# Performance work log

Hardware: AMD Instinct MI355X
Metric: run time of the kernel (lower is better)

Reference implementation:

```python
import jax, jax.numpy as jnp
import numpy as np

N, K, C_IN, OUT = 65536, 16, 64, 64
MID = OUT  # mid_planes = out_planes // 1
S = 8      # share_planes
EPS = 1e-5


def _bn(x, gamma, beta, mean, var):
    # Keras BatchNormalization (inference) over the last (channel) axis.
    return (x - mean) * jax.lax.rsqrt(var + EPS) * gamma + beta


def setup_inputs() -> dict:
    key = jax.random.key(0)
    ks = jax.random.split(key, 12)
    d = {
        'point': jax.random.normal(ks[0], (N, 3), jnp.float32),
        'feat': jax.random.normal(ks[1], (N, C_IN), jnp.float32),
        'idx': jax.random.randint(ks[2], (N, K), 0, N, jnp.int32),
        # linear_q / linear_k / linear_v
        'Wq': jax.random.normal(ks[3], (C_IN, MID), jnp.float32) * 0.05,
        'bq': jnp.zeros((MID,), jnp.float32),
        'Wk': jax.random.normal(ks[4], (C_IN, MID), jnp.float32) * 0.05,
        'bk': jnp.zeros((MID,), jnp.float32),
        'Wv': jax.random.normal(ks[5], (C_IN, OUT), jnp.float32) * 0.05,
        'bv': jnp.zeros((OUT,), jnp.float32),
        # linear_p: Dense(3) -> BN -> ReLU -> Dense(out)
        'p_w1': jax.random.normal(ks[6], (3, 3), jnp.float32) * 0.5,
        'p_b1': jnp.zeros((3,), jnp.float32),
        'p_bn_g': jnp.ones((3,), jnp.float32),
        'p_bn_b': jnp.zeros((3,), jnp.float32),
        'p_bn_m': jnp.zeros((3,), jnp.float32),
        'p_bn_v': jnp.ones((3,), jnp.float32),
        'p_w2': jax.random.normal(ks[7], (3, OUT), jnp.float32) * 0.1,
        'p_b2': jnp.zeros((OUT,), jnp.float32),
        # linear_w: BN -> ReLU -> Dense(mid//s) -> BN -> ReLU -> Dense(out//s)
        'w_bn1_g': jnp.ones((MID,), jnp.float32),
        'w_bn1_b': jnp.zeros((MID,), jnp.float32),
        'w_bn1_m': jnp.zeros((MID,), jnp.float32),
        'w_bn1_v': jnp.ones((MID,), jnp.float32),
        'w_w1': jax.random.normal(ks[8], (MID, MID // S), jnp.float32) * 0.05,
        'w_b1': jnp.zeros((MID // S,), jnp.float32),
        'w_bn2_g': jnp.ones((MID // S,), jnp.float32),
        'w_bn2_b': jnp.zeros((MID // S,), jnp.float32),
        'w_bn2_m': jnp.zeros((MID // S,), jnp.float32),
        'w_bn2_v': jnp.ones((MID // S,), jnp.float32),
        'w_w2': jax.random.normal(ks[9], (MID // S, OUT // S), jnp.float32) * 0.1,
        'w_b2': jnp.zeros((OUT // S,), jnp.float32),
    }
    return d


def reference(point, feat, idx, Wq, bq, Wk, bk, Wv, bv,
              p_w1, p_b1, p_bn_g, p_bn_b, p_bn_m, p_bn_v, p_w2, p_b2,
              w_bn1_g, w_bn1_b, w_bn1_m, w_bn1_v, w_w1, w_b1,
              w_bn2_g, w_bn2_b, w_bn2_m, w_bn2_v, w_w2, w_b2):
    n = point.shape[0]
    feat_q = feat @ Wq + bq                       # (n, mid)
    feat_k = feat @ Wk + bk                       # (n, mid)
    feat_v = feat @ Wv + bv                       # (n, out)
    # queryandgroup: KNN gather + relative positions
    g_xyz = point[idx] - point[:, None, :]        # (n, k, 3)
    g_k = feat_k[idx]                             # (n, k, mid)
    g_v = feat_v[idx]                             # (n, k, out)
    # linear_p MLP on relative positions
    p = g_xyz @ p_w1 + p_b1
    p = jax.nn.relu(_bn(p, p_bn_g, p_bn_b, p_bn_m, p_bn_v))
    p = p @ p_w2 + p_b2                           # (n, k, out)
    # sum over out_planes//mid_planes (= 1) groups, kept for faithfulness
    pr = p.reshape(n, K, OUT // MID, MID).sum(axis=2)  # (n, k, mid)
    # subtraction attention scores
    w = g_k - feat_q[:, None, :] + pr             # (n, k, mid)
    w = jax.nn.relu(_bn(w, w_bn1_g, w_bn1_b, w_bn1_m, w_bn1_v))
    w = w @ w_w1 + w_b1                           # (n, k, mid//s)
    w = jax.nn.relu(_bn(w, w_bn2_g, w_bn2_b, w_bn2_m, w_bn2_v))
    w = w @ w_w2 + w_b2                           # (n, k, out//s)
    # NOTE: original uses Softmax(axis=-1) -> over the out//share channel axis
    w = jax.nn.softmax(w, axis=-1)
    # grouped weighted sum over neighbors
    v = (g_v + p).reshape(n, K, S, OUT // S)      # (n, k, s, out//s)
    out = (v * w[:, :, None, :]).sum(axis=1)      # (n, s, out//s)
    return out.reshape(n, OUT)
```

## Files before the change

kernel.cpp:

```cpp
#include <hip/hip_runtime.h>

typedef unsigned short u16;
typedef unsigned int   u32;
typedef float f32x2 __attribute__((ext_vector_type(2)));

__device__ __forceinline__ u16 f2b(float f) {
    u32 u = __float_as_uint(f);
    return (u16)((u + 0x7fffu + ((u >> 16) & 1u)) >> 16);
}
__device__ __forceinline__ u32 pack2f(float a, float b) {
    return (u32)f2b(a) | ((u32)f2b(b) << 16);
}
__device__ __forceinline__ f32x2 unpk2(u32 w) {
    f32x2 r;
    r[0] = __uint_as_float(w << 16);
    r[1] = __uint_as_float(w & 0xffff0000u);
    return r;
}
__device__ __forceinline__ int permc(int c) { return ((c & 7) << 3) | (c >> 3); }
__device__ __forceinline__ f32x2 bc2(float x) { f32x2 r; r[0] = x; r[1] = x; return r; }
__device__ __forceinline__ f32x2 mk2(float a, float b) { f32x2 r; r[0] = a; r[1] = b; return r; }

__device__ __forceinline__ void dot2bf(float& c, u32 a, u32 b) {
    asm("v_dot2_f32_bf16 %0, %1, %2, %0" : "+v"(c) : "v"(a), "v"(b));
}
__device__ __forceinline__ u32 cvtpk(float lo, float hi) {
    u32 r;
    asm("v_cvt_pk_bf16_f32 %0, %1, %2" : "=v"(r) : "v"(lo), "v"(hi));
    return r;
}

template<int CTRL>
__device__ __forceinline__ float dppf(float x) {
    return __int_as_float(__builtin_amdgcn_update_dpp(0, __float_as_int(x), CTRL, 0xf, 0xf, true));
}
__device__ __forceinline__ float gsum8(float x) {
    x += dppf<0xB1>(x);
    x += dppf<0x4E>(x);
    x += dppf<0x141>(x);
    return x;
}
__device__ __forceinline__ float gmax8(float x) {
    x = fmaxf(x, dppf<0xB1>(x));
    x = fmaxf(x, dppf<0x4E>(x));
    x = fmaxf(x, dppf<0x141>(x));
    return x;
}

__global__ __launch_bounds__(256) void qkv_kernel(
    const float* __restrict__ feat,
    const float* __restrict__ Wq, const float* __restrict__ bq,
    const float* __restrict__ Wk, const float* __restrict__ bk,
    const float* __restrict__ Wv, const float* __restrict__ bv,
    u16* __restrict__ qt, u16* __restrict__ kvt)
{
    __shared__ u32 wpk[3][32][64];
    __shared__ u32 fpk[32][132];
    const int t = threadIdx.x;
    const int rowbase = blockIdx.x * 128;

    {
        const float* Ws[3] = {Wq, Wk, Wv};
#pragma unroll
        for (int mm = 0; mm < 3; mm++) {
            for (int e = t; e < 512; e += 256) {
                int ip = e >> 4, c4 = (e & 15) * 4;
                float4 wa = *(const float4*)&Ws[mm][(2 * ip) * 64 + c4];
                float4 wb = *(const float4*)&Ws[mm][(2 * ip + 1) * 64 + c4];
                wpk[mm][ip][permc(c4 + 0)] = pack2f(wa.x, wb.x);
                wpk[mm][ip][permc(c4 + 1)] = pack2f(wa.y, wb.y);
                wpk[mm][ip][permc(c4 + 2)] = pack2f(wa.z, wb.z);
                wpk[mm][ip][permc(c4 + 3)] = pack2f(wa.w, wb.w);
            }
        }
    }
    for (int e = t; e < 2048; e += 256) {
        int r = e >> 4, ip2 = (e & 15) * 2;
        float4 v = *(const float4*)&feat[(size_t)(rowbase + r) * 64 + ip2 * 2];
        fpk[ip2][r]     = pack2f(v.x, v.y);
        fpk[ip2 + 1][r] = pack2f(v.z, v.w);
    }
    __syncthreads();

    const int rg = t >> 3;
    const int q8 = t & 7;
    const int c0 = q8 * 8;

    float acc[3][4][8];
    {
        const float* Bs[3] = {bq, bk, bv};
#pragma unroll
        for (int m = 0; m < 3; m++)
#pragma unroll
            for (int x = 0; x < 8; x++) {
                float b = Bs[m][x * 8 + q8];
#pragma unroll
                for (int r = 0; r < 4; r++) acc[m][r][x] = b;
            }
    }

#pragma unroll 2
    for (int ip = 0; ip < 32; ip++) {
        uint4 f4 = *(const uint4*)&fpk[ip][rg * 4];
        u32 fr[4] = {f4.x, f4.y, f4.z, f4.w};
#pragma unroll
        for (int m = 0; m < 3; m++) {
            uint4 wv0 = *(const uint4*)&wpk[m][ip][c0];
            uint4 wv1 = *(const uint4*)&wpk[m][ip][c0 + 4];
            u32 wc[8] = {wv0.x, wv0.y, wv0.z, wv0.w, wv1.x, wv1.y, wv1.z, wv1.w};
#pragma unroll
            for (int r = 0; r < 4; r++)
#pragma unroll
                for (int x = 0; x < 8; x++)
                    dot2bf(acc[m][r][x], fr[r], wc[x]);
        }
    }

#pragma unroll
    for (int r = 0; r < 4; r++) {
        int row = rowbase + rg * 4 + r;
        uint4 oq, ok, ov;
        oq.x = cvtpk(acc[0][r][0], acc[0][r][1]); oq.y = cvtpk(acc[0][r][2], acc[0][r][3]);
        oq.z = cvtpk(acc[0][r][4], acc[0][r][5]); oq.w = cvtpk(acc[0][r][6], acc[0][r][7]);
        ok.x = cvtpk(acc[1][r][0], acc[1][r][1]); ok.y = cvtpk(acc[1][r][2], acc[1][r][3]);
        ok.z = cvtpk(acc[1][r][4], acc[1][r][5]); ok.w = cvtpk(acc[1][r][6], acc[1][r][7]);
        ov.x = cvtpk(acc[2][r][0], acc[2][r][1]); ov.y = cvtpk(acc[2][r][2], acc[2][r][3]);
        ov.z = cvtpk(acc[2][r][4], acc[2][r][5]); ov.w = cvtpk(acc[2][r][6], acc[2][r][7]);
        *(uint4*)&qt [(size_t)row * 64 + c0]       = oq;
        *(uint4*)&kvt[(size_t)row * 128 + c0]      = ok;
        *(uint4*)&kvt[(size_t)row * 128 + 64 + c0] = ov;
    }
}

__global__ __launch_bounds__(256) void attn_kernel(
    const float* __restrict__ point,
    const int*   __restrict__ idx,
    const u16*   __restrict__ qt,
    const u16*   __restrict__ kvt,
    const float* __restrict__ p_w1,   const float* __restrict__ p_b1,
    const float* __restrict__ p_bn_g, const float* __restrict__ p_bn_b,
    const float* __restrict__ p_bn_m, const float* __restrict__ p_bn_v,
    const float* __restrict__ p_w2,   const float* __restrict__ p_b2,
    const float* __restrict__ w_bn1_g, const float* __restrict__ w_bn1_b,
    const float* __restrict__ w_bn1_m, const float* __restrict__ w_bn1_v,
    const float* __restrict__ w_w1,    const float* __restrict__ w_b1,
    const float* __restrict__ w_bn2_g, const float* __restrict__ w_bn2_b,
    const float* __restrict__ w_bn2_m, const float* __restrict__ w_bn2_v,
    const float* __restrict__ w_w2,    const float* __restrict__ w_b2,
    float* __restrict__ out)
{
    const int t  = threadIdx.x;
    const int l8 = t & 7;
    const int n  = blockIdx.x * 32 + (t >> 3);
    const float EPS = 1e-5f;

    float pw1[9];
#pragma unroll
    for (int i = 0; i < 9; i++) pw1[i] = p_w1[i];
    float pb1b[3], pbs[3], pbh[3];
#pragma unroll
    for (int a = 0; a < 3; a++) {
        float s = p_bn_g[a] * rsqrtf(p_bn_v[a] + EPS);
        pb1b[a] = p_b1[a];
        pbs[a]  = s;
        pbh[a]  = p_bn_b[a] - p_bn_m[a] * s;
    }
    float b2s[8], b2hh[8];
#pragma unroll
    for (int h = 0; h < 8; h++) {
        float s = w_bn2_g[h] * rsqrtf(w_bn2_v[h] + EPS);
        b2s[h]  = s;
        b2hh[h] = (w_bn2_b[h] - w_bn2_m[h] * s) + w_b1[h] * s;
    }

    f32x2 P0[4], P1[4], P2[4], PB[4];
#pragma unroll
    for (int p = 0; p < 4; p++) {
        int ce = 16 * p + l8, co = ce + 8;
        P0[p] = mk2(p_w2[ce],       p_w2[co]);
        P1[p] = mk2(p_w2[64 + ce],  p_w2[64 + co]);
        P2[p] = mk2(p_w2[128 + ce], p_w2[128 + co]);
        PB[p] = mk2(p_b2[ce],       p_b2[co]);
    }
    u32 W1pk[4][8];
#pragma unroll
    for (int p = 0; p < 4; p++) {
        int ce = 16 * p + l8, co = ce + 8;
        float4 e0 = *(const float4*)&w_w1[ce * 8];
        float4 e1 = *(const float4*)&w_w1[ce * 8 + 4];
        float4 o0 = *(const float4*)&w_w1[co * 8];
        float4 o1 = *(const float4*)&w_w1[co * 8 + 4];
        W1pk[p][0] = pack2f(e0.x, o0.x); W1pk[p][1] = pack2f(e0.y, o0.y);
        W1pk[p][2] = pack2f(e0.z, o0.z); W1pk[p][3] = pack2f(e0.w, o0.w);
        W1pk[p][4] = pack2f(e1.x, o1.x); W1pk[p][5] = pack2f(e1.y, o1.y);
        W1pk[p][6] = pack2f(e1.z, o1.z); W1pk[p][7] = pack2f(e1.w, o1.w);
    }
    u32 ww2pk[4];
#pragma unroll
    for (int i = 0; i < 4; i++)
        ww2pk[i] = pack2f(w_w2[(2 * i) * 8 + l8], w_w2[(2 * i + 1) * 8 + l8]);
    const float wb2l = w_b2[l8];

    f32x2 s2[4], qh2[4];
    {
        uint4 qr = *(const uint4*)&qt[(size_t)n * 64 + l8 * 8];
        const u32* qw = (const u32*)&qr;
#pragma unroll
        for (int p = 0; p < 4; p++) {
            int ce = 16 * p + l8, co = ce + 8;
            float se = w_bn1_g[ce] * rsqrtf(w_bn1_v[ce] + EPS);
            float so = w_bn1_g[co] * rsqrtf(w_bn1_v[co] + EPS);
            float he = w_bn1_b[ce] - w_bn1_m[ce] * se;
            float ho = w_bn1_b[co] - w_bn1_m[co] * so;
            f32x2 q2 = unpk2(qw[p]);
            s2[p]  = mk2(se, so);
            qh2[p] = mk2(he - q2[0] * se, ho - q2[1] * so);
        }
    }

    const float px = point[n * 3], py = point[n * 3 + 1], pz = point[n * 3 + 2];
    f32x2 acc2[4];
#pragma unroll
    for (int p = 0; p < 4; p++) acc2[p] = mk2(0.f, 0.f);

    const int ib = n * 16;
    int j_nxt = idx[ib];
    const u16* kp0 = kvt + (size_t)j_nxt * 128 + l8 * 8;
    uint4 kr = *(const uint4*)kp0;
    uint4 vr = *(const uint4*)(kp0 + 64);
    float2 jxy = *(const float2*)&point[j_nxt * 3];
    float  jz  = point[j_nxt * 3 + 2];
    j_nxt = idx[ib + 1];

#pragma unroll 4
    for (int kk = 0; kk < 16; kk++) {
        int i2 = kk + 2;
        int j_n2 = idx[ib + (i2 < 16 ? i2 : 15)];
        const u16* kpn = kvt + (size_t)j_nxt * 128 + l8 * 8;
        uint4 krn = *(const uint4*)kpn;
        uint4 vrn = *(const uint4*)(kpn + 64);
        float2 jxyn = *(const float2*)&point[j_nxt * 3];
        float  jzn  = point[j_nxt * 3 + 2];

        float dx = jxy.x - px, dy = jxy.y - py, dz = jz - pz;
        float t0 = fmaxf(0.f, fmaf(fmaf(dz, pw1[6], fmaf(dy, pw1[3], fmaf(dx, pw1[0], pb1b[0]))), pbs[0], pbh[0]));
        float t1 = fmaxf(0.f, fmaf(fmaf(dz, pw1[7], fmaf(dy, pw1[4], fmaf(dx, pw1[1], pb1b[1]))), pbs[1], pbh[1]));
        float t2 = fmaxf(0.f, fmaf(fmaf(dz, pw1[8], fmaf(dy, pw1[5], fmaf(dx, pw1[2], pb1b[2]))), pbs[2], pbh[2]));
        f32x2 tp0 = bc2(t0), tp1 = bc2(t1), tp2 = bc2(t2);

        const u32* kw = (const u32*)&kr;
        float partial[8];
#pragma unroll
        for (int h = 0; h < 8; h++) partial[h] = 0.f;
        f32x2 pjs[4];

#pragma unroll
        for (int p = 0; p < 4; p++) {
            f32x2 pj = PB[p] + tp0 * P0[p] + tp1 * P1[p] + tp2 * P2[p];
            pjs[p] = pj;
            f32x2 kf = unpk2(kw[p]);
            f32x2 w2 = (kf + pj) * s2[p] + qh2[p];
            u32 wpk_ = cvtpk(fmaxf(w2[0], 0.f), fmaxf(w2[1], 0.f));
#pragma unroll
            for (int h = 0; h < 8; h++) dot2bf(partial[h], wpk_, W1pk[p][h]);
        }
#pragma unroll
        for (int h = 0; h < 8; h++) partial[h] = gsum8(partial[h]);

        float wb[8];
#pragma unroll
        for (int h = 0; h < 8; h++) wb[h] = fmaxf(0.f, fmaf(partial[h], b2s[h], b2hh[h]));
        float y = wb2l;
#pragma unroll
        for (int i = 0; i < 4; i++) dot2bf(y, cvtpk(wb[2 * i], wb[2 * i + 1]), ww2pk[i]);

        float mx = gmax8(y);
        float e  = __expf(y - mx);
        float ssum = gsum8(e);
        float sm = e * __builtin_amdgcn_rcpf(ssum);
        f32x2 sm2 = bc2(sm);

        const u32* vw = (const u32*)&vr;
#pragma unroll
        for (int p = 0; p < 4; p++) {
            f32x2 vp = unpk2(vw[p]) + pjs[p];
            acc2[p] += sm2 * vp;
        }

        kr = krn; vr = vrn; jxy = jxyn; jz = jzn; j_nxt = j_n2;
    }

#pragma unroll
    for (int p = 0; p < 4; p++) {
        out[(size_t)n * 64 + 16 * p + l8]     = acc2[p][0];
        out[(size_t)n * 64 + 16 * p + 8 + l8] = acc2[p][1];
    }
}

extern "C" void kernel_launch(void* const* d_in, const int* in_sizes, int n_in,
                              void* d_out, int out_size, void* d_ws, size_t ws_size,
                              hipStream_t stream)
{
    const float* point   = (const float*)d_in[0];
    const float* feat    = (const float*)d_in[1];
    const int*   idx     = (const int*)d_in[2];
    const float* Wq      = (const float*)d_in[3];
    const float* bq      = (const float*)d_in[4];
    const float* Wk      = (const float*)d_in[5];
    const float* bk      = (const float*)d_in[6];
    const float* Wv      = (const float*)d_in[7];
    const float* bv      = (const float*)d_in[8];
    const float* p_w1    = (const float*)d_in[9];
    const float* p_b1    = (const float*)d_in[10];
    const float* p_bn_g  = (const float*)d_in[11];
    const float* p_bn_b  = (const float*)d_in[12];
    const float* p_bn_m  = (const float*)d_in[13];
    const float* p_bn_v  = (const float*)d_in[14];
    const float* p_w2    = (const float*)d_in[15];
    const float* p_b2    = (const float*)d_in[16];
    const float* w_bn1_g = (const float*)d_in[17];
    const float* w_bn1_b = (const float*)d_in[18];
    const float* w_bn1_m = (const float*)d_in[19];
    const float* w_bn1_v = (const float*)d_in[20];
    const float* w_w1    = (const float*)d_in[21];
    const float* w_b1    = (const float*)d_in[22];
    const float* w_bn2_g = (const float*)d_in[23];
    const float* w_bn2_b = (const float*)d_in[24];
    const float* w_bn2_m = (const float*)d_in[25];
    const float* w_bn2_v = (const float*)d_in[26];
    const float* w_w2    = (const float*)d_in[27];
    const float* w_b2    = (const float*)d_in[28];
    float* out = (float*)d_out;

    const int N = in_sizes[0] / 3;

    u16* kvt = (u16*)d_ws;
    u16* qt  = (u16*)d_ws + (size_t)N * 128;

    qkv_kernel<<<N / 128, 256, 0, stream>>>(feat, Wq, bq, Wk, bk, Wv, bv, qt, kvt);
    attn_kernel<<<N / 32, 256, 0, stream>>>(point, idx, qt, kvt,
                                            p_w1, p_b1, p_bn_g, p_bn_b, p_bn_m, p_bn_v, p_w2, p_b2,
                                            w_bn1_g, w_bn1_b, w_bn1_m, w_bn1_v, w_w1, w_b1,
                                            w_bn2_g, w_bn2_b, w_bn2_m, w_bn2_v, w_w2, w_b2,
                                            out);
}
```

Baseline: 86.32 us.

## Replace per-head butterfly reductions with transpose-reduce and vectorize neighbor index loads

Eight separate gsum8 reductions over the 8-lane group are replaced by a DPP transpose-reduce. Each lane ends up holding one head's sum, which takes seven DPP adds instead of twenty-four. The W1 and W2 weights are pre-permuted per lane (phi8 xor lane) so that the reduced values and the DPP-broadcast values line up with the correct heads for the second dot product. Neighbor indices are now loaded as int4 vectors and the loop is fully unrolled through a lambda, which cuts scalar index loads but may raise register pressure.

```diff
diff --git a/kernel.cpp b/kernel.cpp
--- a/kernel.cpp
+++ b/kernel.cpp
@@ -46,6 +46,7 @@
     x = fmaxf(x, dppf<0x141>(x));
     return x;
 }
+__device__ __forceinline__ int phi8(int r) { return (r < 4) ? r : (r ^ 3); }
 
 __global__ __launch_bounds__(256) void qkv_kernel(
     const float* __restrict__ feat,
@@ -165,13 +166,6 @@
         pbs[a]  = s;
         pbh[a]  = p_bn_b[a] - p_bn_m[a] * s;
     }
-    float b2s[8], b2hh[8];
-#pragma unroll
-    for (int h = 0; h < 8; h++) {
-        float s = w_bn2_g[h] * rsqrtf(w_bn2_v[h] + EPS);
-        b2s[h]  = s;
-        b2hh[h] = (w_bn2_b[h] - w_bn2_m[h] * s) + w_b1[h] * s;
-    }
 
     f32x2 P0[4], P1[4], P2[4], PB[4];
 #pragma unroll
@@ -186,19 +180,25 @@
 #pragma unroll
     for (int p = 0; p < 4; p++) {
         int ce = 16 * p + l8, co = ce + 8;
-        float4 e0 = *(const float4*)&w_w1[ce * 8];
-        float4 e1 = *(const float4*)&w_w1[ce * 8 + 4];
-        float4 o0 = *(const float4*)&w_w1[co * 8];
-        float4 o1 = *(const float4*)&w_w1[co * 8 + 4];
-        W1pk[p][0] = pack2f(e0.x, o0.x); W1pk[p][1] = pack2f(e0.y, o0.y);
-        W1pk[p][2] = pack2f(e0.z, o0.z); W1pk[p][3] = pack2f(e0.w, o0.w);
-        W1pk[p][4] = pack2f(e1.x, o1.x); W1pk[p][5] = pack2f(e1.y, o1.y);
-        W1pk[p][6] = pack2f(e1.z, o1.z); W1pk[p][7] = pack2f(e1.w, o1.w);
-    }
-    u32 ww2pk[4];
-#pragma unroll
-    for (int i = 0; i < 4; i++)
-        ww2pk[i] = pack2f(w_w2[(2 * i) * 8 + l8], w_w2[(2 * i + 1) * 8 + l8]);
+#pragma unroll
+        for (int r = 0; r < 8; r++) {
+            int hh = phi8(r) ^ l8;
+            W1pk[p][r] = pack2f(w_w1[ce * 8 + hh], w_w1[co * 8 + hh]);
+        }
+    }
+    float b2s_l, b2hh_l;
+    {
+        float s = w_bn2_g[l8] * rsqrtf(w_bn2_v[l8] + EPS);
+        b2s_l  = s;
+        b2hh_l = (w_bn2_b[l8] - w_bn2_m[l8] * s) + w_b1[l8] * s;
+    }
+    u32 ww2xpk[4];
+#pragma unroll
+    for (int i = 0; i < 4; i++) {
+        int h0 = phi8(2 * i)     ^ l8;
+        int h1 = phi8(2 * i + 1) ^ l8;
+        ww2xpk[i] = pack2f(w_w2[h0 * 8 + l8], w_w2[h1 * 8 + l8]);
+    }
     const float wb2l = w_b2[l8];
 
     f32x2 s2[4], qh2[4];
@@ -223,24 +223,16 @@
 #pragma unroll
     for (int p = 0; p < 4; p++) acc2[p] = mk2(0.f, 0.f);
 
-    const int ib = n * 16;
-    int j_nxt = idx[ib];
-    const u16* kp0 = kvt + (size_t)j_nxt * 128 + l8 * 8;
-    uint4 kr = *(const uint4*)kp0;
-    uint4 vr = *(const uint4*)(kp0 + 64);
-    float2 jxy = *(const float2*)&point[j_nxt * 3];
-    float  jz  = point[j_nxt * 3 + 2];
-    j_nxt = idx[ib + 1];
-
-#pragma unroll 4
-    for (int kk = 0; kk < 16; kk++) {
-        int i2 = kk + 2;
-        int j_n2 = idx[ib + (i2 < 16 ? i2 : 15)];
-        const u16* kpn = kvt + (size_t)j_nxt * 128 + l8 * 8;
+    uint4 kr, vr;
+    float2 jxy;
+    float  jz;
+
+    auto proc = [&](int jn) {
+        const u16* kpn = kvt + (size_t)jn * 128 + l8 * 8;
         uint4 krn = *(const uint4*)kpn;
         uint4 vrn = *(const uint4*)(kpn + 64);
-        float2 jxyn = *(const float2*)&point[j_nxt * 3];
-        float  jzn  = point[j_nxt * 3 + 2];
+        float2 jxyn = *(const float2*)&point[jn * 3];
+        float  jzn  = point[jn * 3 + 2];
 
         float dx = jxy.x - px, dy = jxy.y - py, dz = jz - pz;
         float t0 = fmaxf(0.f, fmaf(fmaf(dz, pw1[6], fmaf(dy, pw1[3], fmaf(dx, pw1[0], pb1b[0]))), pbs[0], pbh[0]));
@@ -249,9 +241,9 @@
         f32x2 tp0 = bc2(t0), tp1 = bc2(t1), tp2 = bc2(t2);
 
         const u32* kw = (const u32*)&kr;
-        float partial[8];
-#pragma unroll
-        for (int h = 0; h < 8; h++) partial[h] = 0.f;
+        float part[8];
+#pragma unroll
+        for (int h = 0; h < 8; h++) part[h] = 0.f;
         f32x2 pjs[4];
 
 #pragma unroll
@@ -262,17 +254,28 @@
             f32x2 w2 = (kf + pj) * s2[p] + qh2[p];
             u32 wpk_ = cvtpk(fmaxf(w2[0], 0.f), fmaxf(w2[1], 0.f));
 #pragma unroll
-            for (int h = 0; h < 8; h++) dot2bf(partial[h], wpk_, W1pk[p][h]);
-        }
-#pragma unroll
-        for (int h = 0; h < 8; h++) partial[h] = gsum8(partial[h]);
-
-        float wb[8];
-#pragma unroll
-        for (int h = 0; h < 8; h++) wb[h] = fmaxf(0.f, fmaf(partial[h], b2s[h], b2hh[h]));
+            for (int r = 0; r < 8; r++) dot2bf(part[r], wpk_, W1pk[p][r]);
+        }
+        part[0] += dppf<0xB1>(part[1]);
+        part[2] += dppf<0xB1>(part[3]);
+        part[4] += dppf<0xB1>(part[5]);
+        part[6] += dppf<0xB1>(part[7]);
+        part[0] += dppf<0x4E>(part[2]);
+        part[4] += dppf<0x4E>(part[6]);
+        part[0] += dppf<0x141>(part[4]);
+        float wbl = fmaxf(0.f, fmaf(part[0], b2s_l, b2hh_l));
+        float u1 = dppf<0xB1>(wbl);
+        float u2 = dppf<0x4E>(wbl);
+        float u3 = dppf<0x4E>(u1);
+        float u4 = dppf<0x141>(wbl);
+        float u5 = dppf<0x141>(u1);
+        float u6 = dppf<0x141>(u2);
+        float u7 = dppf<0x141>(u3);
         float y = wb2l;
-#pragma unroll
-        for (int i = 0; i < 4; i++) dot2bf(y, cvtpk(wb[2 * i], wb[2 * i + 1]), ww2pk[i]);
+        dot2bf(y, cvtpk(wbl, u1), ww2xpk[0]);
+        dot2bf(y, cvtpk(u2, u3), ww2xpk[1]);
+        dot2bf(y, cvtpk(u4, u5), ww2xpk[2]);
+        dot2bf(y, cvtpk(u6, u7), ww2xpk[3]);
 
         float mx = gmax8(y);
         float e  = __expf(y - mx);
@@ -287,7 +290,26 @@
             acc2[p] += sm2 * vp;
         }
 
-        kr = krn; vr = vrn; jxy = jxyn; jz = jzn; j_nxt = j_n2;
+        kr = krn; vr = vrn; jxy = jxyn; jz = jzn;
+    };
+
+    const int4* idxq = (const int4*)(idx + n * 16);
+    int4 I = idxq[0];
+    {
+        const u16* kp0 = kvt + (size_t)I.x * 128 + l8 * 8;
+        kr  = *(const uint4*)kp0;
+        vr  = *(const uint4*)(kp0 + 64);
+        jxy = *(const float2*)&point[I.x * 3];
+        jz  = point[I.x * 3 + 2];
+    }
+#pragma unroll
+    for (int kg = 0; kg < 4; kg++) {
+        int4 In = (kg < 3) ? idxq[kg + 1] : I;
+        proc(I.y);
+        proc(I.z);
+        proc(I.w);
+        proc(In.x);
+        I = In;
     }
 
 #pragma unroll
```

Measured after the change: 83.34 us. -3.4%, faster.
